# Optimization experiments

Hardware: AMD Instinct MI355X
Metric: run time of the kernel (lower is better)

The kernel has to match this reference:

```python
import jax, jax.numpy as jnp
import numpy as np

BATCH = 4096
INDIM = 1024
OUTDIM = 1024
NNZ = 52224  # min(1024,1024) * int(1024 * 0.05)


def setup_inputs() -> dict:
    key = jax.random.key(0)
    k1, k2, k3, k4, k5 = jax.random.split(key, 5)
    stdv = np.sqrt(2.0 / INDIM).astype(np.float32)
    input_ = jax.random.normal(k1, (BATCH, INDIM), dtype=jnp.float32)
    weight = jax.random.normal(k2, (NNZ,), dtype=jnp.float32) * stdv
    bias = jax.random.normal(k3, (OUTDIM,), dtype=jnp.float32) * stdv
    ind_in = jax.random.randint(k4, (NNZ,), 0, INDIM, dtype=jnp.int32)
    ind_out = jax.random.randint(k5, (NNZ,), 0, OUTDIM, dtype=jnp.int32)
    return {"input_": input_, "weight": weight, "bias": bias,
            "ind_in": ind_in, "ind_out": ind_out}


def reference(input_, weight, bias, ind_in, ind_out):
    # x = input_[:, ind_in] * weight        [B, NNZ]
    gathered = input_[:, ind_in] * weight
    # scatter_add into output columns       [B, OUTDIM]
    out = jnp.zeros((input_.shape[0], OUTDIM), dtype=input_.dtype)
    out = out.at[:, ind_out].add(gathered)
    return out + bias
```

## Files before the change

kernel.cpp:

```cpp
#include <hip/hip_runtime.h>
#include <stdint.h>

#define INDIM   1024
#define OUTDIM  1024
#define BM 64
#define BN 64
#define BK 128
#define KTILES (INDIM / BK)

typedef __attribute__((ext_vector_type(8))) short  short8;
typedef __attribute__((ext_vector_type(4))) float  floatx4;

__device__ __forceinline__ uint32_t bf16pack(float x, float y) {
    uint32_t ux = __float_as_uint(x);
    ux = ((ux + 0x7FFFu + ((ux >> 16) & 1u)) >> 16) & 0xFFFFu;
    uint32_t uy = __float_as_uint(y);
    uy = (uy + 0x7FFFu + ((uy >> 16) & 1u)) & 0xFFFF0000u;
    return ux | uy;
}

__device__ __forceinline__ uint32_t bf16lo(float x) {
    uint32_t u = __float_as_uint(x);
    return ((u + 0x7FFFu + ((u >> 16) & 1u)) >> 16) & 0xFFFFu;
}

__device__ __forceinline__ void atomic_pk_add_bf16(uint32_t* addr, uint32_t val) {
    asm volatile("global_atomic_pk_add_bf16 %0, %1, off"
                 :: "v"(addr), "v"(val) : "memory");
}

__global__ __launch_bounds__(256) void k_prep(
    const int* __restrict__ ind_in, const int* __restrict__ ind_out,
    const float* __restrict__ wgt, int nnz,
    const float4* __restrict__ A32, int nA4,
    uint32_t* __restrict__ W16T, uint2* __restrict__ A16)
{
    const int gtid   = blockIdx.x * 256 + threadIdx.x;
    const int stride = gridDim.x * 256;

    if (gtid < nnz) {
        const uint32_t idx = ((uint32_t)ind_out[gtid] << 10) | (uint32_t)ind_in[gtid];
        const uint32_t w16 = bf16lo(wgt[gtid]);
        atomic_pk_add_bf16(W16T + (idx >> 1), (idx & 1) ? (w16 << 16) : w16);
    }

    for (int j = gtid; j < nA4; j += stride) {
        float4 v = A32[j];
        A16[j] = make_uint2(bf16pack(v.x, v.y), bf16pack(v.z, v.w));
    }
}

__device__ __forceinline__ void gload_lds16(const ushort* g, ushort* l) {
    __builtin_amdgcn_global_load_lds(
        (const __attribute__((address_space(1))) void*)g,
        (__attribute__((address_space(3))) void*)l, 16, 0, 0);
}

__global__ __launch_bounds__(256, 4) void k_gemm(
    const ushort* __restrict__ A16,
    const ushort* __restrict__ W16T,
    const float* __restrict__ bias,
    float* __restrict__ C, int M)
{
    __shared__ ushort lA[BM * BK];
    __shared__ ushort lB[BN * BK];

    const int t      = threadIdx.x;
    const int w      = t >> 6;
    const int L      = t & 63;
    const int lane15 = L & 15;
    const int quad   = L >> 4;
    const int wm     = w >> 1, wn = w & 1;

    const int bid = blockIdx.x;
    const int bm0 = ((bid & 7) * 8 + (bid >> 7)) * BM;
    const int bn0 = ((bid >> 3) & 15) * BN;

    const int srow = t >> 4;
    const int j8   = (t & 15) ^ (srow & 7);

    const ushort* Abase = A16  + (size_t)bm0 * INDIM;
    const ushort* Bbase = W16T + (size_t)bn0 * INDIM;

    ushort* dA[4], * dB[4];
    #pragma unroll
    for (int q = 0; q < 4; ++q) {
        dA[q] = lA + w * 512 + q * 2048;
        dB[q] = lB + w * 512 + q * 2048;
    }

    floatx4 acc[2][2] = {};

    for (int kt = 0; kt < KTILES; ++kt) {
        const int gcol = kt * BK + j8 * 8;
        __syncthreads();
        #pragma unroll
        for (int q = 0; q < 4; ++q) {
            gload_lds16(Abase + (size_t)(srow + q * 16) * INDIM + gcol, dA[q]);
            gload_lds16(Bbase + (size_t)(srow + q * 16) * INDIM + gcol, dB[q]);
        }
        __syncthreads();

        #pragma unroll
        for (int ks = 0; ks < 4; ++ks) {
            const int j = ks * 4 + quad;
            short8 af[2], bf[2];
            #pragma unroll
            for (int tm = 0; tm < 2; ++tm) {
                const int row = wm * 32 + tm * 16 + lane15;
                af[tm] = *(const short8*)(lA + row * BK + (j ^ (row & 7)) * 8);
            }
            #pragma unroll
            for (int tn = 0; tn < 2; ++tn) {
                const int row = wn * 32 + tn * 16 + lane15;
                bf[tn] = *(const short8*)(lB + row * BK + (j ^ (row & 7)) * 8);
            }
            #pragma unroll
            for (int tm = 0; tm < 2; ++tm)
                #pragma unroll
                for (int tn = 0; tn < 2; ++tn)
                    acc[tm][tn] = __builtin_amdgcn_mfma_f32_16x16x32_bf16(
                        af[tm], bf[tn], acc[tm][tn], 0, 0, 0);
        }
    }

    #pragma unroll
    for (int tm = 0; tm < 2; ++tm) {
        #pragma unroll
        for (int tn = 0; tn < 2; ++tn) {
            const int col = bn0 + wn * 32 + tn * 16 + lane15;
            const float bv = bias[col];
            #pragma unroll
            for (int r = 0; r < 4; ++r) {
                const int row = bm0 + wm * 32 + tm * 16 + quad * 4 + r;
                __builtin_nontemporal_store(acc[tm][tn][r] + bv,
                                            &C[(size_t)row * OUTDIM + col]);
            }
        }
    }
}

extern "C" void kernel_launch(void* const* d_in, const int* in_sizes, int n_in,
                              void* d_out, int out_size, void* d_ws, size_t ws_size,
                              hipStream_t stream) {
    const float* input  = (const float*)d_in[0];
    const float* weight = (const float*)d_in[1];
    const float* bias   = (const float*)d_in[2];
    const int*   ind_in  = (const int*)d_in[3];
    const int*   ind_out = (const int*)d_in[4];
    float* out = (float*)d_out;

    const int nnz = in_sizes[1];
    const int M   = out_size / OUTDIM;
    const int nA4 = M * INDIM / 4;

    char* ws = (char*)d_ws;
    ushort* W16T = (ushort*)ws;
    ushort* A16  = (ushort*)(ws + (2u << 20));

    k_prep<<<2048, 256, 0, stream>>>(ind_in, ind_out, weight, nnz,
                                     (const float4*)input, nA4,
                                     (uint32_t*)W16T, (uint2*)A16);
    k_gemm<<<(M / BM) * (OUTDIM / BN), 256, 0, stream>>>(A16, W16T, bias, out, M);
}
```

Baseline: 93.95 us.

## Double-buffer GEMM LDS tiles with async global-to-LDS prefetch

The GEMM main loop now halves the K tile and keeps two LDS buffers per operand. The next tile is issued with direct global-to-LDS loads before the current tile is computed, and partial vmcnt waits plus barriers let loads overlap MFMA work. This targets the load-then-sync stall of the single-buffered loop. In exchange there are twice as many barrier iterations, and the correctness of the manual waitcnt ordering now depends on exact load counts.

Measured after the change: 92.65 us. No clear change (-1.4%).

```diff
diff --git a/kernel.cpp b/kernel.cpp
--- a/kernel.cpp
+++ b/kernel.cpp
@@ -5,7 +5,7 @@
 #define OUTDIM  1024
 #define BM 64
 #define BN 64
-#define BK 128
+#define BK 64
 #define KTILES (INDIM / BK)
 
 typedef __attribute__((ext_vector_type(8))) short  short8;
@@ -62,8 +62,8 @@
     const float* __restrict__ bias,
     float* __restrict__ C, int M)
 {
-    __shared__ ushort lA[BM * BK];
-    __shared__ ushort lB[BN * BK];
+    __shared__ ushort lA[2][BM * BK];
+    __shared__ ushort lB[2][BN * BK];
 
     const int t      = threadIdx.x;
     const int w      = t >> 6;
@@ -76,44 +76,38 @@
     const int bm0 = ((bid & 7) * 8 + (bid >> 7)) * BM;
     const int bn0 = ((bid >> 3) & 15) * BN;
 
-    const int srow = t >> 4;
-    const int j8   = (t & 15) ^ (srow & 7);
+    const int srow = t >> 3;
+    const int j8   = (t & 7) ^ (srow & 7);
 
-    const ushort* Abase = A16  + (size_t)bm0 * INDIM;
-    const ushort* Bbase = W16T + (size_t)bn0 * INDIM;
+    const ushort* As = A16  + (size_t)(bm0 + srow) * INDIM + j8 * 8;
+    const ushort* Bs = W16T + (size_t)(bn0 + srow) * INDIM + j8 * 8;
 
-    ushort* dA[4], * dB[4];
-    #pragma unroll
-    for (int q = 0; q < 4; ++q) {
-        dA[q] = lA + w * 512 + q * 2048;
-        dB[q] = lB + w * 512 + q * 2048;
-    }
+    const int dbase = w * 512;
+
+    auto STAGE = [&](int buf, int kt) {
+        const int g = kt * BK;
+        gload_lds16(As + g,              &lA[buf][dbase]);
+        gload_lds16(As + g + 32 * INDIM, &lA[buf][dbase + 2048]);
+        gload_lds16(Bs + g,              &lB[buf][dbase]);
+        gload_lds16(Bs + g + 32 * INDIM, &lB[buf][dbase + 2048]);
+    };
 
     floatx4 acc[2][2] = {};
 
-    for (int kt = 0; kt < KTILES; ++kt) {
-        const int gcol = kt * BK + j8 * 8;
-        __syncthreads();
+    auto COMPUTE = [&](int buf) {
         #pragma unroll
-        for (int q = 0; q < 4; ++q) {
-            gload_lds16(Abase + (size_t)(srow + q * 16) * INDIM + gcol, dA[q]);
-            gload_lds16(Bbase + (size_t)(srow + q * 16) * INDIM + gcol, dB[q]);
-        }
-        __syncthreads();
-
-        #pragma unroll
-        for (int ks = 0; ks < 4; ++ks) {
+        for (int ks = 0; ks < 2; ++ks) {
             const int j = ks * 4 + quad;
             short8 af[2], bf[2];
             #pragma unroll
             for (int tm = 0; tm < 2; ++tm) {
                 const int row = wm * 32 + tm * 16 + lane15;
-                af[tm] = *(const short8*)(lA + row * BK + (j ^ (row & 7)) * 8);
+                af[tm] = *(const short8*)(&lA[buf][row * BK + ((j ^ (row & 7)) << 3)]);
             }
             #pragma unroll
             for (int tn = 0; tn < 2; ++tn) {
                 const int row = wn * 32 + tn * 16 + lane15;
-                bf[tn] = *(const short8*)(lB + row * BK + (j ^ (row & 7)) * 8);
+                bf[tn] = *(const short8*)(&lB[buf][row * BK + ((j ^ (row & 7)) << 3)]);
             }
             #pragma unroll
             for (int tm = 0; tm < 2; ++tm)
@@ -122,7 +116,23 @@
                     acc[tm][tn] = __builtin_amdgcn_mfma_f32_16x16x32_bf16(
                         af[tm], bf[tn], acc[tm][tn], 0, 0, 0);
         }
+    };
+
+    STAGE(0, 0);
+    #pragma unroll 2
+    for (int kt = 0; kt < KTILES - 1; ++kt) {
+        STAGE((kt + 1) & 1, kt + 1);
+        asm volatile("s_waitcnt vmcnt(4)" ::: "memory");
+        __builtin_amdgcn_s_barrier();
+        __builtin_amdgcn_sched_barrier(0);
+        COMPUTE(kt & 1);
+        __builtin_amdgcn_sched_barrier(0);
+        __builtin_amdgcn_s_barrier();
     }
+    asm volatile("s_waitcnt vmcnt(0)" ::: "memory");
+    __builtin_amdgcn_s_barrier();
+    __builtin_amdgcn_sched_barrier(0);
+    COMPUTE((KTILES - 1) & 1);
 
     #pragma unroll
     for (int tm = 0; tm < 2; ++tm) {
```

## Pre-swizzle A and W into MFMA fragment layout and drop LDS staging

Applied to the files above, without the earlier changes.

The prep kernel now writes both the bf16 input and the densified weight directly in a 16x32 fragment-tiled layout that matches the MFMA operand order. The GEMM then loads each wave's fragments straight from global memory with one contiguous 16-byte load per lane and no shared memory or barriers. The aim is to remove the LDS round trip and the __syncthreads stalls. In exchange, operands shared by waves and blocks are re-read through cache instead of from LDS, and the prep stores become more scattered.

New measurement: 101.8 us. +8.4%, slower.

```diff
diff --git a/kernel.cpp b/kernel.cpp
--- a/kernel.cpp
+++ b/kernel.cpp
@@ -5,8 +5,6 @@
 #define OUTDIM  1024
 #define BM 64
 #define BN 64
-#define BK 128
-#define KTILES (INDIM / BK)
 
 typedef __attribute__((ext_vector_type(8))) short  short8;
 typedef __attribute__((ext_vector_type(4))) float  floatx4;
@@ -32,39 +30,41 @@
 __global__ __launch_bounds__(256) void k_prep(
     const int* __restrict__ ind_in, const int* __restrict__ ind_out,
     const float* __restrict__ wgt, int nnz,
-    const float4* __restrict__ A32, int nA4,
-    uint32_t* __restrict__ W16T, uint2* __restrict__ A16)
+    const float* __restrict__ A32, int M,
+    uint32_t* __restrict__ W16F, uint32_t* __restrict__ A16F)
 {
-    const int gtid   = blockIdx.x * 256 + threadIdx.x;
-    const int stride = gridDim.x * 256;
+    const int g = blockIdx.x * 256 + threadIdx.x;
 
-    if (gtid < nnz) {
-        const uint32_t idx = ((uint32_t)ind_out[gtid] << 10) | (uint32_t)ind_in[gtid];
-        const uint32_t w16 = bf16lo(wgt[gtid]);
-        atomic_pk_add_bf16(W16T + (idx >> 1), (idx & 1) ? (w16 << 16) : w16);
+    if (g < nnz) {
+        const int k = ind_in[g], n = ind_out[g];
+        const uint32_t off = ((uint32_t)(n >> 4) * 32 + (uint32_t)(k >> 5)) * 512
+                           + (((uint32_t)(k >> 3) & 3u) << 7)
+                           + (((uint32_t)n & 15u) << 3) + ((uint32_t)k & 7u);
+        const uint32_t w16 = bf16lo(wgt[g]);
+        atomic_pk_add_bf16(W16F + (off >> 1), (k & 1) ? (w16 << 16) : w16);
     }
 
-    for (int j = gtid; j < nA4; j += stride) {
-        float4 v = A32[j];
-        A16[j] = make_uint2(bf16pack(v.x, v.y), bf16pack(v.z, v.w));
+    const int nG = M * (INDIM / 8);
+    for (int j = g; j < nG; j += gridDim.x * 256) {
+        const int m = j >> 7, k0 = (j & 127) << 3;
+        const float4 v0 = *(const float4*)(A32 + (size_t)m * INDIM + k0);
+        const float4 v1 = *(const float4*)(A32 + (size_t)m * INDIM + k0 + 4);
+        uint4 o;
+        o.x = bf16pack(v0.x, v0.y); o.y = bf16pack(v0.z, v0.w);
+        o.z = bf16pack(v1.x, v1.y); o.w = bf16pack(v1.z, v1.w);
+        const uint32_t off = ((uint32_t)(m >> 4) * 32 + (uint32_t)(k0 >> 5)) * 512
+                           + (((uint32_t)(k0 >> 3) & 3u) << 7)
+                           + (((uint32_t)m & 15u) << 3);
+        *(uint4*)(A16F + (off >> 1)) = o;
     }
 }
 
-__device__ __forceinline__ void gload_lds16(const ushort* g, ushort* l) {
-    __builtin_amdgcn_global_load_lds(
-        (const __attribute__((address_space(1))) void*)g,
-        (__attribute__((address_space(3))) void*)l, 16, 0, 0);
-}
-
 __global__ __launch_bounds__(256, 4) void k_gemm(
-    const ushort* __restrict__ A16,
-    const ushort* __restrict__ W16T,
+    const ushort* __restrict__ A16F,
+    const ushort* __restrict__ W16F,
     const float* __restrict__ bias,
     float* __restrict__ C, int M)
 {
-    __shared__ ushort lA[BM * BK];
-    __shared__ ushort lB[BN * BK];
-
     const int t      = threadIdx.x;
     const int w      = t >> 6;
     const int L      = t & 63;
@@ -73,57 +73,33 @@
     const int wm     = w >> 1, wn = w & 1;
 
     const int bid = blockIdx.x;
-    const int bm0 = ((bid & 7) * 8 + (bid >> 7)) * BM;
-    const int bn0 = ((bid >> 3) & 15) * BN;
+    const int mb  = (bid & 7) * 8 + (bid >> 7);
+    const int nb  = (bid >> 3) & 15;
 
-    const int srow = t >> 4;
-    const int j8   = (t & 15) ^ (srow & 7);
+    const int bmt = mb * 4 + wm * 2;
+    const int bnt = nb * 4 + wn * 2;
 
-    const ushort* Abase = A16  + (size_t)bm0 * INDIM;
-    const ushort* Bbase = W16T + (size_t)bn0 * INDIM;
-
-    ushort* dA[4], * dB[4];
-    #pragma unroll
-    for (int q = 0; q < 4; ++q) {
-        dA[q] = lA + w * 512 + q * 2048;
-        dB[q] = lB + w * 512 + q * 2048;
-    }
+    const ushort* pA0 = A16F + (size_t)(bmt    ) * 32 * 512 + L * 8;
+    const ushort* pA1 = A16F + (size_t)(bmt + 1) * 32 * 512 + L * 8;
+    const ushort* pB0 = W16F + (size_t)(bnt    ) * 32 * 512 + L * 8;
+    const ushort* pB1 = W16F + (size_t)(bnt + 1) * 32 * 512 + L * 8;
 
     floatx4 acc[2][2] = {};
 
-    for (int kt = 0; kt < KTILES; ++kt) {
-        const int gcol = kt * BK + j8 * 8;
-        __syncthreads();
-        #pragma unroll
-        for (int q = 0; q < 4; ++q) {
-            gload_lds16(Abase + (size_t)(srow + q * 16) * INDIM + gcol, dA[q]);
-            gload_lds16(Bbase + (size_t)(srow + q * 16) * INDIM + gcol, dB[q]);
-        }
-        __syncthreads();
-
-        #pragma unroll
-        for (int ks = 0; ks < 4; ++ks) {
-            const int j = ks * 4 + quad;
-            short8 af[2], bf[2];
-            #pragma unroll
-            for (int tm = 0; tm < 2; ++tm) {
-                const int row = wm * 32 + tm * 16 + lane15;
-                af[tm] = *(const short8*)(lA + row * BK + (j ^ (row & 7)) * 8);
-            }
-            #pragma unroll
-            for (int tn = 0; tn < 2; ++tn) {
-                const int row = wn * 32 + tn * 16 + lane15;
-                bf[tn] = *(const short8*)(lB + row * BK + (j ^ (row & 7)) * 8);
-            }
-            #pragma unroll
-            for (int tm = 0; tm < 2; ++tm)
-                #pragma unroll
-                for (int tn = 0; tn < 2; ++tn)
-                    acc[tm][tn] = __builtin_amdgcn_mfma_f32_16x16x32_bf16(
-                        af[tm], bf[tn], acc[tm][tn], 0, 0, 0);
-        }
+    #pragma unroll 4
+    for (int kk = 0; kk < 32; ++kk) {
+        const short8 a0 = *(const short8*)(pA0 + kk * 512);
+        const short8 a1 = *(const short8*)(pA1 + kk * 512);
+        const short8 b0 = *(const short8*)(pB0 + kk * 512);
+        const short8 b1 = *(const short8*)(pB1 + kk * 512);
+        acc[0][0] = __builtin_amdgcn_mfma_f32_16x16x32_bf16(a0, b0, acc[0][0], 0, 0, 0);
+        acc[0][1] = __builtin_amdgcn_mfma_f32_16x16x32_bf16(a0, b1, acc[0][1], 0, 0, 0);
+        acc[1][0] = __builtin_amdgcn_mfma_f32_16x16x32_bf16(a1, b0, acc[1][0], 0, 0, 0);
+        acc[1][1] = __builtin_amdgcn_mfma_f32_16x16x32_bf16(a1, b1, acc[1][1], 0, 0, 0);
     }
 
+    const int bm0 = mb * 64;
+    const int bn0 = nb * 64;
     #pragma unroll
     for (int tm = 0; tm < 2; ++tm) {
         #pragma unroll
@@ -152,14 +128,12 @@
 
     const int nnz = in_sizes[1];
     const int M   = out_size / OUTDIM;
-    const int nA4 = M * INDIM / 4;
 
     char* ws = (char*)d_ws;
-    ushort* W16T = (ushort*)ws;
-    ushort* A16  = (ushort*)(ws + (2u << 20));
+    ushort* W16F = (ushort*)ws;
+    ushort* A16F = (ushort*)(ws + (2u << 20));
 
     k_prep<<<2048, 256, 0, stream>>>(ind_in, ind_out, weight, nnz,
-                                     (const float4*)input, nA4,
-                                     (uint32_t*)W16T, (uint2*)A16);
-    k_gemm<<<(M / BM) * (OUTDIM / BN), 256, 0, stream>>>(A16, W16T, bias, out, M);
+                                     input, M, (uint32_t*)W16F, (uint32_t*)A16F);
+    k_gemm<<<(M / BM) * (OUTDIM / BN), 256, 0, stream>>>(A16F, W16F, bias, out, M);
 }
```
